# Kernel optimization log

Hardware: AMD Instinct MI355X
Metric: run time of the kernel (lower is better)

Reference implementation:

```python
import jax, jax.numpy as jnp
import numpy as np

NUM_HEADS = 16
INNER = 128      # per-head q/k dim
OUT = 128        # per-head v dim
D_MODEL = 1024
SEQ = 2048
MASK_SCALE = -1000000000.0  # ENSURE_MASKED_IS_ZERO


def setup_inputs() -> dict:
    key = jax.random.key(0)
    ks = jax.random.split(key, 8)
    scale = 1.0 / np.sqrt(D_MODEL)
    inputs = jax.random.normal(ks[0], (SEQ, D_MODEL), dtype=jnp.float32)
    sequence_mask = jax.random.bernoulli(ks[1], 0.5, (SEQ,))
    Wq = jax.random.normal(ks[2], (D_MODEL, NUM_HEADS * INNER), dtype=jnp.float32) * scale
    bq = jnp.zeros((NUM_HEADS * INNER,), dtype=jnp.float32)
    Wk = jax.random.normal(ks[3], (D_MODEL, NUM_HEADS * INNER), dtype=jnp.float32) * scale
    bk = jnp.zeros((NUM_HEADS * INNER,), dtype=jnp.float32)
    Wv = jax.random.normal(ks[4], (D_MODEL, NUM_HEADS * OUT), dtype=jnp.float32) * scale
    bv = jnp.zeros((NUM_HEADS * OUT,), dtype=jnp.float32)
    return {"inputs": inputs, "sequence_mask": sequence_mask,
            "Wq": Wq, "bq": bq, "Wk": Wk, "bk": bk, "Wv": Wv, "bv": bv}


def reference(inputs, sequence_mask, Wq, bq, Wk, bk, Wv, bv):
    S = inputs.shape[0]
    # Dense projections, then split heads; vmap(in_axes=1) in the original == head-major layout [H, S, D]
    q = (inputs @ Wq + bq).reshape(S, NUM_HEADS, INNER).transpose(1, 0, 2)
    k = (inputs @ Wk + bk).reshape(S, NUM_HEADS, INNER).transpose(1, 0, 2)
    v = (inputs @ Wv + bv).reshape(S, NUM_HEADS, OUT).transpose(1, 0, 2)
    # raw scores / sqrt(d_k)
    scores = jnp.einsum('hsd,htd->hst', q, k) / jnp.sqrt(jnp.float32(INNER))
    # Faithful to original: scores are MULTIPLIED by the mask matrix
    # mask = outer(m, m) * (-1e9): -1e9 where both positions True, 0 otherwise.
    mask = (sequence_mask[:, None] & sequence_mask[None, :]).astype(scores.dtype) * MASK_SCALE
    scores = scores * mask  # broadcast over head axis
    attn = jax.nn.softmax(scores, axis=-1)           # [H, S, S]
    out = jnp.einsum('hst,htd->hsd', attn, v)        # [H, S, OUT]
    return out.transpose(1, 0, 2).reshape(S, NUM_HEADS * OUT)
```

## Files before the change

### kernel.cpp

```cpp
#include <hip/hip_runtime.h>
#include <hip/hip_bf16.h>
#include <cfloat>
#include <math.h>

typedef __bf16 bf16;
typedef __bf16 bf16x4 __attribute__((ext_vector_type(4)));
typedef __bf16 bf16x8 __attribute__((ext_vector_type(8)));
typedef float  floatx4 __attribute__((ext_vector_type(4)));
typedef float  floatx2 __attribute__((ext_vector_type(2)));

#define SEQ 2048
#define DM  1024
#define NP  2048
#define CAP (1 << 20)
#define MARGIN 0.5f
#define LBUF 1024

__device__ __forceinline__ unsigned enc_f(float f) {
  unsigned b = __float_as_uint(f);
  return ((int)b >= 0) ? (b | 0x80000000u) : ~b;
}
__device__ __forceinline__ float dec_f(unsigned u) {
  return (u & 0x80000000u) ? __uint_as_float(u & 0x7fffffffu) : __uint_as_float(~u);
}

__global__ __launch_bounds__(256) void mask_prep(
    const void* __restrict__ mraw, int* __restrict__ maskw,
    int* __restrict__ midx, int* __restrict__ mc,
    int* __restrict__ gcount, float* __restrict__ sums,
    unsigned long long* __restrict__ keys, unsigned* __restrict__ gmin) {
  int t = threadIdx.x;
  if (blockIdx.x > 0) {
    int b = blockIdx.x - 1;
    for (int j = 0; j < 4; j++) {
      int i = b * 1024 + j * 256 + t;
      keys[i] = ~0ULL;
      gmin[i] = 0xFFFFFFFFu;
    }
    if (b == 0) for (int i = t; i < 2048; i += 256) sums[i] = 0.f;
    return;
  }
  __shared__ int flags;
  __shared__ int lmask[2048];
  if (t == 0) { flags = 0; *gcount = 0; }
  __syncthreads();
  const unsigned short* u16 = (const unsigned short*)mraw;
  const unsigned* u32 = (const unsigned*)mraw;
  int f = 0;
  for (int i = t; i < 1024; i += 256) {
    unsigned short v = u16[i];
    if (v != 0 && v != 0x3F80u) f |= 1;
    if ((i & 1) == 0 && v == 0x3F80u) f |= 2;
  }
  for (int i = t; i < 512; i += 256)
    if (u32[i] > 1u) f |= 4;
  if (f) atomicOr(&flags, f);
  __syncthreads();
  int fl = flags;
  int mode;
  if (!(fl & 1)) mode = (fl & 2) ? 2 : 3;
  else           mode = (fl & 4) ? 1 : 0;
  for (int s = t; s < SEQ; s += 256) {
    int m;
    if (mode == 0)      m = (((const int*)mraw)[s] != 0);
    else if (mode == 1) m = (((const unsigned char*)mraw)[s] != 0);
    else if (mode == 2) m = (u16[s] != 0);
    else                m = (((const float*)mraw)[s] != 0.0f);
    maskw[s] = m; lmask[s] = m;
  }
  __syncthreads();
  if (t < 64) {
    int base = 0;
    for (int c = 0; c < 32; c++) {
      int s = c * 64 + t;
      bool m = lmask[s] != 0;
      unsigned long long bal = __ballot(m);
      if (m) midx[base + __popcll(bal & ((1ULL << t) - 1ULL))] = s;
      base += __popcll(bal);
    }
    if (t == 0) *mc = base;
  }
}

__global__ __launch_bounds__(256) void split_x(
    const float* __restrict__ X,
    bf16* __restrict__ Xh, bf16* __restrict__ Xm) {
  int i = blockIdx.x * 256 + threadIdx.x;
  floatx4 v = *(const floatx4*)(X + (size_t)i * 4);
  bf16x4 hv, mv;
  #pragma unroll
  for (int j = 0; j < 4; j++) {
    float x = v[j];
    bf16 h = (bf16)x; float r1 = x - (float)h;
    hv[j] = h; mv[j] = (bf16)r1;
  }
  *(bf16x4*)(Xh + (size_t)i * 4) = hv;
  *(bf16x4*)(Xm + (size_t)i * 4) = mv;
}

__global__ __launch_bounds__(256) void split_w(
    const float* __restrict__ Wq, const float* __restrict__ Wk,
    const float* __restrict__ Wv,
    bf16* __restrict__ Tqh, bf16* __restrict__ Tqm,
    bf16* __restrict__ Tkh, bf16* __restrict__ Tkm,
    bf16* __restrict__ Tvh) {
  int z = blockIdx.z;
  const float* W = (z == 0) ? Wq : (z == 1) ? Wk : Wv;
  bf16* Th = (z == 0) ? Tqh : (z == 1) ? Tkh : Tvh;
  bf16* Tm = (z == 0) ? Tqm : Tkm;
  __shared__ float tile[32][33];
  int n0 = blockIdx.x * 32, k0 = blockIdx.y * 32;
  int t = threadIdx.x, r = t >> 3, c4 = (t & 7) * 4;
  floatx4 v = *(const floatx4*)(W + (size_t)(k0 + r) * NP + n0 + c4);
  tile[r][c4 + 0] = v[0]; tile[r][c4 + 1] = v[1];
  tile[r][c4 + 2] = v[2]; tile[r][c4 + 3] = v[3];
  __syncthreads();
  bf16x4 hv, mv;
  #pragma unroll
  for (int j = 0; j < 4; j++) {
    float x = tile[c4 + j][r];
    bf16 h = (bf16)x; float r1 = x - (float)h;
    hv[j] = h; mv[j] = (bf16)r1;
  }
  size_t base = (size_t)(n0 + r) * DM + k0 + c4;
  *(bf16x4*)(Th + base) = hv;
  if (z < 2)
    *(bf16x4*)(Tm + base) = mv;
}

__global__ __launch_bounds__(256) void proj_qk3(
    const bf16* __restrict__ Xh, const bf16* __restrict__ Xm,
    const bf16* __restrict__ Qh_, const bf16* __restrict__ Qm_,
    const bf16* __restrict__ Kh_, const bf16* __restrict__ Km_,
    const float* __restrict__ bq, const float* __restrict__ bk,
    const int* __restrict__ midx, const int* __restrict__ mc,
    float* __restrict__ qf, float* __restrict__ kf,
    bf16* __restrict__ qbf, bf16* __restrict__ kbf) {
  int mcv = *mc;
  int lin = blockIdx.x;
  int z    = lin & 1;
  int head = (lin >> 1) & 15;
  int ms   = (lin >> 5) * 64;
  if (mcv == 0 || ms >= mcv) return;
  const bf16* WTh = z ? Kh_ : Qh_;
  const bf16* WTm = z ? Km_ : Qm_;
  const float* bia = z ? bk : bq;
  float* outf = z ? kf : qf;
  bf16*  outb = z ? kbf : qbf;
  int ns = head * 128;
  __shared__ alignas(16) bf16 Ah[64][40], Am[64][40];
  __shared__ alignas(16) bf16 Bh[128][40], Bm[128][40];
  int t = threadIdx.x, w = t >> 6, lane = t & 63, l15 = lane & 15, qd = lane >> 4;
  int wm = (w & 1) * 32, wn = (w >> 1) * 64;
  int amr = t >> 2, akb = (t & 3) * 8;
  int bnr = t >> 1, bkb = (t & 1) * 16;
  int cr = ms + amr;
  size_t arow = (size_t)midx[cr < mcv ? cr : (mcv - 1)] * DM + akb;
  const bf16* xhp = Xh + arow;
  const bf16* xmp = Xm + arow;
  const bf16* bhp = WTh + (size_t)(ns + bnr) * DM + bkb;
  const bf16* bmp = WTm + (size_t)(ns + bnr) * DM + bkb;

  floatx4 acc[2][4];
  for (int i = 0; i < 2; i++)
    for (int j = 0; j < 4; j++) acc[i][j] = (floatx4){0.f, 0.f, 0.f, 0.f};

  bf16x8 pa[2], pb[4];
  pa[0] = *(const bf16x8*)(xhp);
  pa[1] = *(const bf16x8*)(xmp);
  pb[0] = *(const bf16x8*)(bhp);     pb[1] = *(const bf16x8*)(bhp + 8);
  pb[2] = *(const bf16x8*)(bmp);     pb[3] = *(const bf16x8*)(bmp + 8);

  for (int kt = 0; kt < DM; kt += 32) {
    __syncthreads();
    *(bf16x8*)&Ah[amr][akb] = pa[0];
    *(bf16x8*)&Am[amr][akb] = pa[1];
    *(bf16x8*)&Bh[bnr][bkb]     = pb[0];
    *(bf16x8*)&Bh[bnr][bkb + 8] = pb[1];
    *(bf16x8*)&Bm[bnr][bkb]     = pb[2];
    *(bf16x8*)&Bm[bnr][bkb + 8] = pb[3];
    __syncthreads();
    if (kt + 32 < DM) {
      int k2 = kt + 32;
      pa[0] = *(const bf16x8*)(xhp + k2);
      pa[1] = *(const bf16x8*)(xmp + k2);
      pb[0] = *(const bf16x8*)(bhp + k2);     pb[1] = *(const bf16x8*)(bhp + k2 + 8);
      pb[2] = *(const bf16x8*)(bmp + k2);     pb[3] = *(const bf16x8*)(bmp + k2 + 8);
    }
    bf16x8 fah[2], fam[2], fbh[4], fbm[4];
    #pragma unroll
    for (int i = 0; i < 2; i++) {
      fah[i] = *(const bf16x8*)&Ah[wm + i * 16 + l15][qd * 8];
      fam[i] = *(const bf16x8*)&Am[wm + i * 16 + l15][qd * 8];
    }
    #pragma unroll
    for (int j = 0; j < 4; j++) {
      fbh[j] = *(const bf16x8*)&Bh[wn + j * 16 + l15][qd * 8];
      fbm[j] = *(const bf16x8*)&Bm[wn + j * 16 + l15][qd * 8];
    }
    #pragma unroll
    for (int i = 0; i < 2; i++)
      #pragma unroll
      for (int j = 0; j < 4; j++) {
        floatx4 a = acc[i][j];
        a = __builtin_amdgcn_mfma_f32_16x16x32_bf16(fam[i], fbh[j], a, 0, 0, 0);
        a = __builtin_amdgcn_mfma_f32_16x16x32_bf16(fah[i], fbm[j], a, 0, 0, 0);
        a = __builtin_amdgcn_mfma_f32_16x16x32_bf16(fah[i], fbh[j], a, 0, 0, 0);
        acc[i][j] = a;
      }
  }
  #pragma unroll
  for (int i = 0; i < 2; i++)
    #pragma unroll
    for (int j = 0; j < 4; j++) {
      int col = wn + j * 16 + l15;
      float bb = bia[ns + col];
      #pragma unroll
      for (int r = 0; r < 4; r++) {
        int row = ms + wm + i * 16 + qd * 4 + r;
        float v = acc[i][j][r] + bb;
        size_t idx = ((size_t)head * SEQ + row) * 128 + col;
        outf[idx] = v;
        outb[idx] = (bf16)v;
      }
    }
}

__global__ __launch_bounds__(256) void proj_v_mfma(
    const bf16* __restrict__ Xh, const bf16* __restrict__ Wvh,
    const float* __restrict__ bia, float* __restrict__ out,
    float* __restrict__ sums) {
  __shared__ alignas(16) bf16 As[64][40];
  __shared__ alignas(16) bf16 Bs[128][40];
  __shared__ float colsum[128];
  int lin = blockIdx.x;
  int ns = (lin & 15) * 128;
  int ms = (lin >> 4) * 64;
  int t = threadIdx.x, w = t >> 6, lane = t & 63, l15 = lane & 15, qd = lane >> 4;
  int wm = (w & 1) * 32, wn = (w >> 1) * 64;
  int amr = t >> 2, akb = (t & 3) * 8;
  int bnr = t >> 1, bkb = (t & 1) * 16;
  if (t < 128) colsum[t] = 0.f;
  const bf16* ap = Xh  + (size_t)(ms + amr) * DM + akb;
  const bf16* bp = Wvh + (size_t)(ns + bnr) * DM + bkb;
  floatx4 acc[2][4];
  for (int i = 0; i < 2; i++)
    for (int j = 0; j < 4; j++) acc[i][j] = (floatx4){0.f, 0.f, 0.f, 0.f};

  bf16x8 pa, pb[2];
  pa    = *(const bf16x8*)(ap);
  pb[0] = *(const bf16x8*)(bp);  pb[1] = *(const bf16x8*)(bp + 8);

  for (int kt = 0; kt < DM; kt += 32) {
    __syncthreads();
    *(bf16x8*)&As[amr][akb]     = pa;
    *(bf16x8*)&Bs[bnr][bkb]     = pb[0];
    *(bf16x8*)&Bs[bnr][bkb + 8] = pb[1];
    __syncthreads();
    if (kt + 32 < DM) {
      int k2 = kt + 32;
      pa    = *(const bf16x8*)(ap + k2);
      pb[0] = *(const bf16x8*)(bp + k2);  pb[1] = *(const bf16x8*)(bp + k2 + 8);
    }
    bf16x8 af[2], bfr[4];
    #pragma unroll
    for (int i = 0; i < 2; i++) af[i]  = *(const bf16x8*)&As[wm + i * 16 + l15][qd * 8];
    #pragma unroll
    for (int j = 0; j < 4; j++) bfr[j] = *(const bf16x8*)&Bs[wn + j * 16 + l15][qd * 8];
    #pragma unroll
    for (int i = 0; i < 2; i++)
      #pragma unroll
      for (int j = 0; j < 4; j++)
        acc[i][j] = __builtin_amdgcn_mfma_f32_16x16x32_bf16(af[i], bfr[j], acc[i][j], 0, 0, 0);
  }
  float part[4] = {0.f, 0.f, 0.f, 0.f};
  for (int i = 0; i < 2; i++) {
    for (int j = 0; j < 4; j++) {
      int n = ns + wn + j * 16 + l15;
      float bb = bia[n];
      for (int r = 0; r < 4; r++) {
        int m = ms + wm + i * 16 + qd * 4 + r;
        float v = acc[i][j][r] + bb;
        out[(size_t)m * NP + n] = v;
        part[j] += v;
      }
    }
  }
  for (int j = 0; j < 4; j++)
    atomicAdd(&colsum[wn + j * 16 + l15], part[j]);
  __syncthreads();
  if (t < 128) atomicAdd(&sums[ns + t], colsum[t]);
}

__global__ __launch_bounds__(256) void scores_min(
    const bf16* __restrict__ Qb, const bf16* __restrict__ Kb,
    const int* __restrict__ mc,
    unsigned* __restrict__ gmin) {
  int mcv = *mc;
  int h = blockIdx.x, s0 = blockIdx.y * 64;
  if (s0 >= mcv) return;
  int ntiles = (mcv + 63) >> 6;
  int half = (ntiles + 1) >> 1;
  int tbeg = blockIdx.z * half;
  int tend = ntiles < tbeg + half ? ntiles : tbeg + half;
  __shared__ alignas(16) bf16 qs[64][136];
  __shared__ alignas(16) bf16 ks[64][136];
  __shared__ float lmin[64][4];
  int t = threadIdx.x, w = t >> 6, lane = t & 63, l15 = lane & 15, qd = lane >> 4;
  const bf16* Qh = Qb + (size_t)h * SEQ * 128;
  const bf16* Kh = Kb + (size_t)h * SEQ * 128;
  int sr = t >> 4, sseg = (t & 15) * 8;
  #pragma unroll
  for (int j = 0; j < 4; j++)
    *(bf16x8*)&qs[sr + j * 16][sseg] = *(const bf16x8*)(Qh + (size_t)(s0 + sr + j * 16) * 128 + sseg);
  bf16x8 pre[4];
  #pragma unroll
  for (int j = 0; j < 4; j++)
    pre[j] = *(const bf16x8*)(Kh + (size_t)(tbeg * 64 + sr + j * 16) * 128 + sseg);
  __syncthreads();
  bf16x8 af[4][4];
  for (int ksp = 0; ksp < 4; ksp++)
    for (int i = 0; i < 4; i++)
      af[ksp][i] = *(const bf16x8*)&qs[i * 16 + l15][ksp * 32 + qd * 8];
  float rmin[4][4];
  for (int i = 0; i < 4; i++)
    for (int r = 0; r < 4; r++) rmin[i][r] = INFINITY;

  for (int tt = tbeg; tt < tend; tt++) {
    __syncthreads();
    #pragma unroll
    for (int j = 0; j < 4; j++)
      *(bf16x8*)&ks[sr + j * 16][sseg] = pre[j];
    __syncthreads();
    if (tt + 1 < tend) {
      #pragma unroll
      for (int j = 0; j < 4; j++)
        pre[j] = *(const bf16x8*)(Kh + (size_t)((tt + 1) * 64 + sr + j * 16) * 128 + sseg);
    }
    floatx4 acc[4];
    for (int i = 0; i < 4; i++) acc[i] = (floatx4){0.f, 0.f, 0.f, 0.f};
    for (int ksp = 0; ksp < 4; ksp++) {
      bf16x8 bfr = *(const bf16x8*)&ks[w * 16 + l15][ksp * 32 + qd * 8];
      for (int i = 0; i < 4; i++)
        acc[i] = __builtin_amdgcn_mfma_f32_16x16x32_bf16(af[ksp][i], bfr, acc[i], 0, 0, 0);
    }
    bool okc = (tt * 64 + w * 16 + l15) < mcv;
    for (int i = 0; i < 4; i++)
      for (int r = 0; r < 4; r++)
        rmin[i][r] = fminf(rmin[i][r], okc ? acc[i][r] : INFINITY);
  }
  for (int m = 1; m < 16; m <<= 1)
    for (int i = 0; i < 4; i++)
      for (int r = 0; r < 4; r++)
        rmin[i][r] = fminf(rmin[i][r], __shfl_xor(rmin[i][r], m));
  if (l15 == 0)
    for (int i = 0; i < 4; i++)
      for (int r = 0; r < 4; r++)
        lmin[i * 16 + qd * 4 + r][w] = rmin[i][r];
  __syncthreads();
  if (t < 64) {
    int row = s0 + t;
    if (row < mcv) {
      float cm = fminf(fminf(lmin[t][0], lmin[t][1]), fminf(lmin[t][2], lmin[t][3]));
      atomicMin(&gmin[h * 2048 + row], enc_f(cm));
    }
  }
}

__global__ __launch_bounds__(256) void scores_collect(
    const bf16* __restrict__ Qb, const bf16* __restrict__ Kb,
    const int* __restrict__ mc, const unsigned* __restrict__ gmin,
    unsigned* __restrict__ cand, int* __restrict__ gcount) {
  int mcv = *mc;
  int h = blockIdx.x, s0 = blockIdx.y * 64;
  if (s0 >= mcv) return;
  int ntiles = (mcv + 63) >> 6;
  int half = (ntiles + 1) >> 1;
  int tbeg = blockIdx.z * half;
  int tend = ntiles < tbeg + half ? ntiles : tbeg + half;
  __shared__ alignas(16) bf16 qs[64][136];
  __shared__ alignas(16) bf16 ks[64][136];
  __shared__ float fmin[64];
  __shared__ unsigned lbuf[LBUF];
  __shared__ int lcount;
  __shared__ int gbase;
  int t = threadIdx.x, w = t >> 6, lane = t & 63, l15 = lane & 15, qd = lane >> 4;
  const bf16* Qh = Qb + (size_t)h * SEQ * 128;
  const bf16* Kh = Kb + (size_t)h * SEQ * 128;
  int sr = t >> 4, sseg = (t & 15) * 8;
  if (t == 0) lcount = 0;
  #pragma unroll
  for (int j = 0; j < 4; j++)
    *(bf16x8*)&qs[sr + j * 16][sseg] = *(const bf16x8*)(Qh + (size_t)(s0 + sr + j * 16) * 128 + sseg);
  bf16x8 pre[4];
  #pragma unroll
  for (int j = 0; j < 4; j++)
    pre[j] = *(const bf16x8*)(Kh + (size_t)(tbeg * 64 + sr + j * 16) * 128 + sseg);
  if (t < 64) {
    int row = s0 + t;
    fmin[t] = (row < mcv) ? dec_f(gmin[h * 2048 + row]) + MARGIN : -INFINITY;
  }
  __syncthreads();
  bf16x8 af[4][4];
  for (int ksp = 0; ksp < 4; ksp++)
    for (int i = 0; i < 4; i++)
      af[ksp][i] = *(const bf16x8*)&qs[i * 16 + l15][ksp * 32 + qd * 8];
  float fm[4][4];
  for (int i = 0; i < 4; i++)
    for (int r = 0; r < 4; r++) fm[i][r] = fmin[i * 16 + qd * 4 + r];

  for (int tt = tbeg; tt < tend; tt++) {
    __syncthreads();
    #pragma unroll
    for (int j = 0; j < 4; j++)
      *(bf16x8*)&ks[sr + j * 16][sseg] = pre[j];
    __syncthreads();
    if (tt + 1 < tend) {
      #pragma unroll
      for (int j = 0; j < 4; j++)
        pre[j] = *(const bf16x8*)(Kh + (size_t)((tt + 1) * 64 + sr + j * 16) * 128 + sseg);
    }
    floatx4 acc[4];
    for (int i = 0; i < 4; i++) acc[i] = (floatx4){0.f, 0.f, 0.f, 0.f};
    for (int ksp = 0; ksp < 4; ksp++) {
      bf16x8 bfr = *(const bf16x8*)&ks[w * 16 + l15][ksp * 32 + qd * 8];
      for (int i = 0; i < 4; i++)
        acc[i] = __builtin_amdgcn_mfma_f32_16x16x32_bf16(af[ksp][i], bfr, acc[i], 0, 0, 0);
    }
    int tg = tt * 64 + w * 16 + l15;
    if (tg < mcv) {
      for (int i = 0; i < 4; i++)
        for (int r = 0; r < 4; r++) {
          if (acc[i][r] <= fm[i][r]) {
            int rr = i * 16 + qd * 4 + r;
            unsigned enc = ((unsigned)h << 22) | ((unsigned)(s0 + rr) << 11) | (unsigned)tg;
            int lp = atomicAdd(&lcount, 1);
            if (lp < LBUF) {
              lbuf[lp] = enc;
            } else {
              int pos = atomicAdd(gcount, 1);
              if (pos < CAP) cand[pos] = enc;
            }
          }
        }
    }
  }
  __syncthreads();
  int cnt = lcount; if (cnt > LBUF) cnt = LBUF;
  if (t == 0) gbase = atomicAdd(gcount, cnt);
  __syncthreads();
  int base = gbase;
  for (int i = t; i < cnt; i += 256) {
    int pos = base + i;
    if (pos < CAP) cand[pos] = lbuf[i];
  }
}

__global__ __launch_bounds__(256) void rescore(
    const float* __restrict__ Q, const float* __restrict__ K,
    const int* __restrict__ midx,
    const unsigned* __restrict__ cand, const int* __restrict__ gcount,
    unsigned long long* __restrict__ keys) {
  int wid  = (blockIdx.x * 256 + threadIdx.x) >> 6;
  int lane = threadIdx.x & 63;
  int nw = gridDim.x * 4;
  int n = *gcount; if (n > CAP) n = CAP;
  for (int c = wid; c < n; c += nw) {
    unsigned u = cand[c];
    int h = u >> 22, cs = (u >> 11) & 2047, ct = u & 2047;
    floatx2 qv = *(const floatx2*)(Q + ((size_t)h * SEQ + cs) * 128 + lane * 2);
    floatx2 kv = *(const floatx2*)(K + ((size_t)h * SEQ + ct) * 128 + lane * 2);
    double d = (double)qv[0] * (double)kv[0] + (double)qv[1] * (double)kv[1];
    for (int off = 32; off; off >>= 1) d += __shfl_down(d, off);
    if (lane == 0) {
      int sorig = midx[cs], torig = midx[ct];
      long long b = __double_as_longlong(d);
      unsigned long long ub = (b >= 0) ? ((unsigned long long)b | 0x8000000000000000ULL)
                                       : ~(unsigned long long)b;
      unsigned long long key = (ub & ~2047ULL) | (unsigned long long)torig;
      atomicMin(&keys[(size_t)h * SEQ + sorig], key);
    }
  }
}

__global__ __launch_bounds__(256) void assemble(
    const float* __restrict__ V, const float* __restrict__ sums,
    const int* __restrict__ mask, const unsigned long long* __restrict__ keys,
    float* __restrict__ out) {
  int idx = blockIdx.x * 256 + threadIdx.x;
  int s = idx >> 11, n = idx & 2047, h = n >> 7;
  float val;
  if (mask[s]) {
    int tt = (int)(keys[(size_t)h * SEQ + s] & 2047ULL);
    val = V[(size_t)tt * NP + n];
  } else {
    val = sums[n] * (1.0f / 2048.0f);
  }
  out[idx] = val;
}

extern "C" void kernel_launch(void* const* d_in, const int* in_sizes, int n_in,
                              void* d_out, int out_size, void* d_ws, size_t ws_size,
                              hipStream_t stream) {
  (void)in_sizes; (void)n_in; (void)out_size; (void)ws_size;
  const float* X    = (const float*)d_in[0];
  const void*  mraw = d_in[1];
  const float* Wq   = (const float*)d_in[2];
  const float* bq   = (const float*)d_in[3];
  const float* Wk   = (const float*)d_in[4];
  const float* bk   = (const float*)d_in[5];
  const float* Wv   = (const float*)d_in[6];
  const float* bv   = (const float*)d_in[7];

  char* ws = (char*)d_ws;
  float* qf  = (float*)ws;
  float* kf  = (float*)(ws + ((size_t)16 << 20));
  bf16*  qbf = (bf16*) (ws + ((size_t)32 << 20));
  bf16*  kbf = (bf16*) (ws + ((size_t)40 << 20));
  bf16* wqh = (bf16*)(ws + ((size_t)48 << 20));
  bf16* wqm = (bf16*)(ws + ((size_t)52 << 20));
  bf16* wkh = (bf16*)(ws + ((size_t)56 << 20));
  bf16* wkm = (bf16*)(ws + ((size_t)60 << 20));
  float* vf = (float*)(ws + ((size_t)48 << 20));
  unsigned* cand = (unsigned*)(ws + ((size_t)64 << 20));
  char* misc = ws + ((size_t)72 << 20);
  int*   maskw  = (int*)misc;
  int*   midx   = (int*)(misc + (8 << 10));
  int*   mc     = (int*)(misc + (16 << 10));
  int*   gcount = (int*)(misc + (16 << 10) + 64);
  float* sums   = (float*)(misc + (32 << 10));
  unsigned long long* keys = (unsigned long long*)(misc + (64 << 10));
  unsigned* gmin = (unsigned*)(misc + (320 << 10));
  bf16* xh  = (bf16*)(ws + ((size_t)73 << 20));
  bf16* xm  = (bf16*)(ws + ((size_t)77 << 20));
  bf16* tvh = (bf16*)(ws + ((size_t)85 << 20));
  float* out = (float*)d_out;

  mask_prep<<<33, 256, 0, stream>>>(mraw, maskw, midx, mc, gcount, sums, keys, gmin);
  split_x<<<2048, 256, 0, stream>>>(X, xh, xm);
  split_w<<<dim3(64, 32, 3), 256, 0, stream>>>(Wq, Wk, Wv, wqh, wqm, wkh, wkm, tvh);
  proj_qk3<<<1024, 256, 0, stream>>>(xh, xm, wqh, wqm, wkh, wkm,
                                     bq, bk, midx, mc, qf, kf, qbf, kbf);
  proj_v_mfma<<<512, 256, 0, stream>>>(xh, tvh, bv, vf, sums);
  scores_min<<<dim3(16, 32, 2), 256, 0, stream>>>(qbf, kbf, mc, gmin);
  scores_collect<<<dim3(16, 32, 2), 256, 0, stream>>>(qbf, kbf, mc, gmin, cand, gcount);
  rescore<<<512, 256, 0, stream>>>(qf, kf, midx, cand, gcount, keys);
  assemble<<<16384, 256, 0, stream>>>(vf, sums, maskw, keys, out);
}
```

Before: 218.0 us.

## Compute V column sums via X-sum matvec and project V only for masked rows

The unmasked-row output (the mean of V over all rows) is now computed algebraically as colsum(X)·Wv plus the bias, using two small reduction kernels. That removes the need to project V for every row. The V projection then runs only on the compacted masked rows (gathered through midx), and the assemble step maps token indices through a new inverse index. This roughly halves the V GEMM work in exchange for two extra small fp32 kernel launches and a gather on the A-tile loads.

After: 262.3 us. +20.3%, slower.

```diff
diff --git a/kernel.cpp b/kernel.cpp
--- a/kernel.cpp
+++ b/kernel.cpp
@@ -26,8 +26,8 @@
 
 __global__ __launch_bounds__(256) void mask_prep(
     const void* __restrict__ mraw, int* __restrict__ maskw,
-    int* __restrict__ midx, int* __restrict__ mc,
-    int* __restrict__ gcount, float* __restrict__ sums,
+    int* __restrict__ midx, int* __restrict__ inv, int* __restrict__ mc,
+    int* __restrict__ gcount, float* __restrict__ sums, float* __restrict__ xsum,
     unsigned long long* __restrict__ keys, unsigned* __restrict__ gmin) {
   int t = threadIdx.x;
   if (blockIdx.x > 0) {
@@ -38,6 +38,7 @@
       gmin[i] = 0xFFFFFFFFu;
     }
     if (b == 0) for (int i = t; i < 2048; i += 256) sums[i] = 0.f;
+    if (b == 1) for (int i = t; i < 1024; i += 256) xsum[i] = 0.f;
     return;
   }
   __shared__ int flags;
@@ -75,7 +76,11 @@
       int s = c * 64 + t;
       bool m = lmask[s] != 0;
       unsigned long long bal = __ballot(m);
-      if (m) midx[base + __popcll(bal & ((1ULL << t) - 1ULL))] = s;
+      if (m) {
+        int ci = base + __popcll(bal & ((1ULL << t) - 1ULL));
+        midx[ci] = s;
+        inv[s] = ci;
+      }
       base += __popcll(bal);
     }
     if (t == 0) *mc = base;
@@ -126,6 +131,32 @@
   *(bf16x4*)(Th + base) = hv;
   if (z < 2)
     *(bf16x4*)(Tm + base) = mv;
+}
+
+__global__ __launch_bounds__(256) void xsum_k(
+    const float* __restrict__ X, float* __restrict__ xsum) {
+  int b = blockIdx.x;
+  int jc = b & 3, jr = b >> 2;
+  int col = jc * 256 + threadIdx.x;
+  float acc = 0.f;
+  int m0 = jr * 64;
+  for (int m = m0; m < m0 + 64; m++)
+    acc += X[(size_t)m * DM + col];
+  atomicAdd(&xsum[col], acc);
+}
+
+__global__ __launch_bounds__(256) void vsum_mv(
+    const float* __restrict__ Wv, const float* __restrict__ xsum,
+    float* __restrict__ sums) {
+  int b = blockIdx.x;
+  int jn = b & 7, jk = b >> 3;
+  int col = jn * 256 + threadIdx.x;
+  float acc = 0.f;
+  int k0 = jk * 128;
+  #pragma unroll 4
+  for (int k = k0; k < k0 + 128; k++)
+    acc += xsum[k] * Wv[(size_t)k * NP + col];
+  atomicAdd(&sums[col], acc);
 }
 
 __global__ __launch_bounds__(256) void proj_qk3(
@@ -228,20 +259,23 @@
 
 __global__ __launch_bounds__(256) void proj_v_mfma(
     const bf16* __restrict__ Xh, const bf16* __restrict__ Wvh,
-    const float* __restrict__ bia, float* __restrict__ out,
-    float* __restrict__ sums) {
+    const float* __restrict__ bia,
+    const int* __restrict__ midx, const int* __restrict__ mc,
+    float* __restrict__ out) {
   __shared__ alignas(16) bf16 As[64][40];
   __shared__ alignas(16) bf16 Bs[128][40];
-  __shared__ float colsum[128];
+  int mcv = *mc;
   int lin = blockIdx.x;
   int ns = (lin & 15) * 128;
   int ms = (lin >> 4) * 64;
+  if (mcv == 0 || ms >= mcv) return;
   int t = threadIdx.x, w = t >> 6, lane = t & 63, l15 = lane & 15, qd = lane >> 4;
   int wm = (w & 1) * 32, wn = (w >> 1) * 64;
   int amr = t >> 2, akb = (t & 3) * 8;
   int bnr = t >> 1, bkb = (t & 1) * 16;
-  if (t < 128) colsum[t] = 0.f;
-  const bf16* ap = Xh  + (size_t)(ms + amr) * DM + akb;
+  int cr = ms + amr;
+  size_t arow = (size_t)midx[cr < mcv ? cr : (mcv - 1)] * DM + akb;
+  const bf16* ap = Xh  + arow;
   const bf16* bp = Wvh + (size_t)(ns + bnr) * DM + bkb;
   floatx4 acc[2][4];
   for (int i = 0; i < 2; i++)
@@ -273,23 +307,15 @@
       for (int j = 0; j < 4; j++)
         acc[i][j] = __builtin_amdgcn_mfma_f32_16x16x32_bf16(af[i], bfr[j], acc[i][j], 0, 0, 0);
   }
-  float part[4] = {0.f, 0.f, 0.f, 0.f};
-  for (int i = 0; i < 2; i++) {
+  for (int i = 0; i < 2; i++)
     for (int j = 0; j < 4; j++) {
       int n = ns + wn + j * 16 + l15;
       float bb = bia[n];
       for (int r = 0; r < 4; r++) {
         int m = ms + wm + i * 16 + qd * 4 + r;
-        float v = acc[i][j][r] + bb;
-        out[(size_t)m * NP + n] = v;
-        part[j] += v;
+        out[(size_t)m * NP + n] = acc[i][j][r] + bb;
       }
     }
-  }
-  for (int j = 0; j < 4; j++)
-    atomicAdd(&colsum[wn + j * 16 + l15], part[j]);
-  __syncthreads();
-  if (t < 128) atomicAdd(&sums[ns + t], colsum[t]);
 }
 
 __global__ __launch_bounds__(256) void scores_min(
@@ -485,16 +511,18 @@
 
 __global__ __launch_bounds__(256) void assemble(
     const float* __restrict__ V, const float* __restrict__ sums,
-    const int* __restrict__ mask, const unsigned long long* __restrict__ keys,
+    const float* __restrict__ bv,
+    const int* __restrict__ mask, const int* __restrict__ inv,
+    const unsigned long long* __restrict__ keys,
     float* __restrict__ out) {
   int idx = blockIdx.x * 256 + threadIdx.x;
   int s = idx >> 11, n = idx & 2047, h = n >> 7;
   float val;
   if (mask[s]) {
     int tt = (int)(keys[(size_t)h * SEQ + s] & 2047ULL);
-    val = V[(size_t)tt * NP + n];
+    val = V[(size_t)inv[tt] * NP + n];
   } else {
-    val = sums[n] * (1.0f / 2048.0f);
+    val = sums[n] * (1.0f / 2048.0f) + bv[n];
   }
   out[idx] = val;
 }
@@ -531,19 +559,23 @@
   float* sums   = (float*)(misc + (32 << 10));
   unsigned long long* keys = (unsigned long long*)(misc + (64 << 10));
   unsigned* gmin = (unsigned*)(misc + (320 << 10));
+  int*   inv    = (int*)(misc + (448 << 10));
+  float* xsum   = (float*)(misc + (456 << 10));
   bf16* xh  = (bf16*)(ws + ((size_t)73 << 20));
   bf16* xm  = (bf16*)(ws + ((size_t)77 << 20));
   bf16* tvh = (bf16*)(ws + ((size_t)85 << 20));
   float* out = (float*)d_out;
 
-  mask_prep<<<33, 256, 0, stream>>>(mraw, maskw, midx, mc, gcount, sums, keys, gmin);
+  mask_prep<<<33, 256, 0, stream>>>(mraw, maskw, midx, inv, mc, gcount, sums, xsum, keys, gmin);
   split_x<<<2048, 256, 0, stream>>>(X, xh, xm);
   split_w<<<dim3(64, 32, 3), 256, 0, stream>>>(Wq, Wk, Wv, wqh, wqm, wkh, wkm, tvh);
+  xsum_k<<<128, 256, 0, stream>>>(X, xsum);
+  vsum_mv<<<64, 256, 0, stream>>>(Wv, xsum, sums);
   proj_qk3<<<1024, 256, 0, stream>>>(xh, xm, wqh, wqm, wkh, wkm,
                                      bq, bk, midx, mc, qf, kf, qbf, kbf);
-  proj_v_mfma<<<512, 256, 0, stream>>>(xh, tvh, bv, vf, sums);
+  proj_v_mfma<<<512, 256, 0, stream>>>(xh, tvh, bv, midx, mc, vf);
   scores_min<<<dim3(16, 32, 2), 256, 0, stream>>>(qbf, kbf, mc, gmin);
   scores_collect<<<dim3(16, 32, 2), 256, 0, stream>>>(qbf, kbf, mc, gmin, cand, gcount);
   rescore<<<512, 256, 0, stream>>>(qf, kf, midx, cand, gcount, keys);
-  assemble<<<16384, 256, 0, stream>>>(vf, sums, maskw, keys, out);
-}
+  assemble<<<16384, 256, 0, stream>>>(vf, sums, bv, maskw, inv, keys, out);
+}
```
